# Kernel tuning notes

Hardware: AMD Instinct MI355X
Metric: run time of the kernel (lower is better)

The kernel has to match this reference:

```python
import jax, jax.numpy as jnp
import numpy as np

B, T, C = 8, 2048, 1024
EXP = 4
EPS = 1e-6


def rmsnorm(x, w):
    xf = x.astype(jnp.float32)
    y = xf * jax.lax.rsqrt(jnp.mean(xf * xf, axis=-1, keepdims=True) + EPS)
    return y.astype(x.dtype) * w


def setup_inputs() -> dict:
    key = jax.random.key(0)
    ks = jax.random.split(key, 8)
    x = jax.random.normal(ks[0], (B, T, C), dtype=jnp.float32)
    norm1_w = jnp.ones((C,), jnp.float32)
    norm2_w = jnp.ones((C,), jnp.float32)
    s1 = 1.0 / np.sqrt(C)
    s2 = 1.0 / np.sqrt(EXP * C)
    mlp1_w = jax.random.uniform(ks[1], (C, C), jnp.float32, -s1, s1)  # stored (in,out)
    mlp1_b = jax.random.uniform(ks[2], (C,), jnp.float32, -s1, s1)
    mlp2_w1 = jax.random.uniform(ks[3], (C, EXP * C), jnp.float32, -s1, s1)
    mlp2_b1 = jax.random.uniform(ks[4], (EXP * C,), jnp.float32, -s1, s1)
    mlp2_w2 = jax.random.uniform(ks[5], (EXP * C, C), jnp.float32, -s2, s2)
    mlp2_b2 = jax.random.uniform(ks[6], (C,), jnp.float32, -s2, s2)
    return {"x": x, "norm1_w": norm1_w, "mlp1_w": mlp1_w, "mlp1_b": mlp1_b,
            "norm2_w": norm2_w, "mlp2_w1": mlp2_w1, "mlp2_b1": mlp2_b1,
            "mlp2_w2": mlp2_w2, "mlp2_b2": mlp2_b2}


def reference(x, norm1_w, mlp1_w, mlp1_b, norm2_w, mlp2_w1, mlp2_b1, mlp2_w2, mlp2_b2):
    Tdim = x.shape[-2]
    # linear-RNN cumulative state with triangular-number scaler (faithful to source)
    state = jnp.cumsum(rmsnorm(x, norm1_w), axis=1)
    scaler = jnp.cumsum(jnp.arange(1, Tdim + 1, dtype=x.dtype))[None, :, None]
    state = state / scaler
    gate = jax.nn.sigmoid(jnp.einsum('btc,cd->btd', state, mlp1_w) + mlp1_b)
    out = gate * x
    h = rmsnorm(out, norm2_w)
    h = jax.nn.relu(jnp.einsum('btc,ce->bte', h, mlp2_w1) + mlp2_b1)
    out = jnp.einsum('bte,ec->btc', h, mlp2_w2) + mlp2_b2 + out
    return out
```

## Files before the change

### kernel.cpp

```cpp
#include <hip/hip_runtime.h>

__device__ __forceinline__ float bf2f(unsigned short u) {
    union { unsigned int i; float f; } v;
    v.i = ((unsigned int)u) << 16;
    return v.f;
}
__device__ __forceinline__ unsigned short f2bf(float f) {
    union { float f; unsigned int i; } v;
    v.f = f;
    unsigned int r = (v.i + 0x7fffu + ((v.i >> 16) & 1u)) >> 16;
    return (unsigned short)r;
}

typedef __attribute__((ext_vector_type(8))) short short8;
typedef __attribute__((ext_vector_type(4))) float floatx4;

#define GLOBAL_AS __attribute__((address_space(1)))
#define LDS_AS __attribute__((address_space(3)))

static constexpr int Bdim = 8;
static constexpr int Tdim = 2048;
static constexpr int Cdim = 1024;
static constexpr int Edim = 4096;
static constexpr int Mdim = Bdim * Tdim;

__global__ __launch_bounds__(256) void transpose_f2b(
    const float* __restrict__ src, unsigned short* __restrict__ dst, int K, int N) {
    __shared__ float tile[32][33];
    int n0 = blockIdx.x * 32;
    int k0 = blockIdx.y * 32;
    int tx = threadIdx.x & 31;
    int ty = threadIdx.x >> 5;
#pragma unroll
    for (int i = 0; i < 32; i += 8)
        tile[ty + i][tx] = src[(size_t)(k0 + ty + i) * N + n0 + tx];
    __syncthreads();
#pragma unroll
    for (int i = 0; i < 32; i += 8)
        dst[(size_t)(n0 + ty + i) * K + k0 + tx] = f2bf(tile[tx][ty + i]);
}

__global__ __launch_bounds__(256) void rms_inv_kernel(
    const float* __restrict__ x, float* __restrict__ rinv) {
    int row = blockIdx.x;
    int tid = threadIdx.x;
    float4 v = ((const float4*)(x + (size_t)row * Cdim))[tid];
    float s = v.x * v.x + v.y * v.y + v.z * v.z + v.w * v.w;
#pragma unroll
    for (int o = 32; o > 0; o >>= 1) s += __shfl_down(s, o, 64);
    __shared__ float ps[4];
    if ((tid & 63) == 0) ps[tid >> 6] = s;
    __syncthreads();
    if (tid == 0) {
        float tot = ps[0] + ps[1] + ps[2] + ps[3];
        rinv[row] = rsqrtf(tot * (1.0f / (float)Cdim) + 1e-6f);
    }
}

__global__ __launch_bounds__(256) void chunk_sums(
    const float* __restrict__ x, const float* __restrict__ rinv,
    const float* __restrict__ w, float* __restrict__ P) {
    int idx = blockIdx.x;
    int cb = idx & 3;
    int k = (idx >> 2) & 31;
    int b = idx >> 7;
    int c = cb * 256 + threadIdx.x;
    float wc = w[c];
    const float* base = x + ((size_t)b * Tdim + k * 64) * Cdim + c;
    const float* rbase = rinv + (size_t)b * Tdim + k * 64;
    float s = 0.f;
#pragma unroll 8
    for (int t = 0; t < 64; t++) s += base[(size_t)t * Cdim] * rbase[t];
    P[((size_t)b * 32 + k) * Cdim + c] = s * wc;
}

__global__ __launch_bounds__(256) void chunk_scan(float* __restrict__ P) {
    int g = blockIdx.x * 256 + threadIdx.x;
    int b = g >> 10;
    int c = g & 1023;
    float* p = P + (size_t)b * 32 * Cdim + c;
    float run = 0.f;
#pragma unroll
    for (int k = 0; k < 32; k++) {
        float v = p[(size_t)k * Cdim];
        p[(size_t)k * Cdim] = run;
        run += v;
    }
}

__global__ __launch_bounds__(256) void cumsum_state(
    const float* __restrict__ x, const float* __restrict__ rinv,
    const float* __restrict__ w, const float* __restrict__ P,
    unsigned short* __restrict__ state) {
    int idx = blockIdx.x;
    int cb = idx & 3;
    int k = (idx >> 2) & 31;
    int b = idx >> 7;
    int c = cb * 256 + threadIdx.x;
    float wc = w[c];
    float acc = P[((size_t)b * 32 + k) * Cdim + c];
    const float* base = x + ((size_t)b * Tdim + k * 64) * Cdim + c;
    const float* rbase = rinv + (size_t)b * Tdim + k * 64;
    unsigned short* sbase = state + ((size_t)b * Tdim + k * 64) * Cdim + c;
#pragma unroll 4
    for (int t = 0; t < 64; t++) {
        acc += base[(size_t)t * Cdim] * rbase[t] * wc;
        int tt = k * 64 + t;
        float inv = 2.0f / ((float)(tt + 1) * (float)(tt + 2));
        sbase[(size_t)t * Cdim] = f2bf(acc * inv);
    }
}

__global__ __launch_bounds__(256) void rmsnorm_f2b(
    const float* __restrict__ x, const float* __restrict__ w,
    unsigned short* __restrict__ y) {
    int row = blockIdx.x;
    int tid = threadIdx.x;
    float4 v = ((const float4*)(x + (size_t)row * Cdim))[tid];
    float s = v.x * v.x + v.y * v.y + v.z * v.z + v.w * v.w;
#pragma unroll
    for (int o = 32; o > 0; o >>= 1) s += __shfl_down(s, o, 64);
    __shared__ float ps[4];
    if ((tid & 63) == 0) ps[tid >> 6] = s;
    __syncthreads();
    float tot = ps[0] + ps[1] + ps[2] + ps[3];
    float r = rsqrtf(tot * (1.0f / (float)Cdim) + 1e-6f);
    float4 w4 = ((const float4*)w)[tid];
    ushort4 o;
    o.x = f2bf(v.x * r * w4.x);
    o.y = f2bf(v.y * r * w4.y);
    o.z = f2bf(v.z * r * w4.z);
    o.w = f2bf(v.w * r * w4.w);
    ((ushort4*)(y + (size_t)row * Cdim))[tid] = o;
}

template <int EPI>
__global__ __launch_bounds__(512, 2) void gemm8(
    const unsigned short* __restrict__ A, const unsigned short* __restrict__ BT,
    const float* __restrict__ bias, const float* __restrict__ extra,
    void* __restrict__ Coutv, int N, int K) {
    __shared__ __attribute__((aligned(16))) unsigned short As[3][256 * 64];
    __shared__ __attribute__((aligned(16))) unsigned short Bs[3][128 * 64];

    int tid = threadIdx.x;
    int nbn = N >> 7;
    int id = blockIdx.x;
    int nwg = gridDim.x;
    if ((nwg & 7) == 0) id = (id & 7) * (nwg >> 3) + (id >> 3);
    int bn = id % nbn;
    int bm = id / nbn;

    int lane = tid & 63;
    int w = tid >> 6;
    int wm = w & 3;
    int wn = w >> 2;
    int lrow = lane & 15;
    int l4 = lane >> 4;
    int swz = lrow & 7;

    const unsigned short* Abase = A + (size_t)bm * 256 * K;
    const unsigned short* Bbase = BT + (size_t)bn * 128 * K;

    int sr = tid >> 3;
    int col8 = (tid & 7) ^ (sr & 7);

#define STAGE_A(sb, u, k0)                                                               \
    __builtin_amdgcn_global_load_lds(                                                    \
        (const GLOBAL_AS void*)(Abase + (size_t)((u) * 64 + sr) * K + (k0) + col8 * 8),  \
        (LDS_AS void*)(As[sb] + (u) * 4096 + tid * 8), 16, 0, 0)
#define STAGE_B(sb, u, k0)                                                               \
    __builtin_amdgcn_global_load_lds(                                                    \
        (const GLOBAL_AS void*)(Bbase + (size_t)((u) * 64 + sr) * K + (k0) + col8 * 8),  \
        (LDS_AS void*)(Bs[sb] + (u) * 4096 + tid * 8), 16, 0, 0)

    floatx4 acc[4][4] = {};
    int nt = K >> 6;

    STAGE_A(0, 0, 0); STAGE_A(0, 1, 0); STAGE_A(0, 2, 0); STAGE_A(0, 3, 0);
    STAGE_B(0, 0, 0); STAGE_B(0, 1, 0);
    STAGE_A(1, 0, 64); STAGE_A(1, 1, 64); STAGE_A(1, 2, 64); STAGE_A(1, 3, 64);
    STAGE_B(1, 0, 64); STAGE_B(1, 1, 64);
    asm volatile("s_waitcnt vmcnt(6)" ::: "memory");
    __builtin_amdgcn_s_barrier();

    int buf = 0;
    for (int t = 0; t < nt; t++) {
        const unsigned short* Ab = As[buf];
        const unsigned short* Bb = Bs[buf];
        int sb = buf + 2; if (sb >= 3) sb -= 3;
        int k2 = (t + 2) << 6;
        bool st = (t + 2) < nt;

        short8 af[4][2], bfr[2][2];
#pragma unroll
        for (int i = 0; i < 4; i++)
#pragma unroll
            for (int ks = 0; ks < 2; ks++)
                af[i][ks] = *(const short8*)(Ab + (wm * 64 + i * 16 + lrow) * 64 +
                                             (((ks * 4 + l4) ^ swz) << 3));
#pragma unroll
        for (int j = 0; j < 2; j++)
#pragma unroll
            for (int ks = 0; ks < 2; ks++)
                bfr[j][ks] = *(const short8*)(Bb + (wn * 64 + j * 16 + lrow) * 64 +
                                              (((ks * 4 + l4) ^ swz) << 3));
        if (st) { STAGE_A(sb, 0, k2); STAGE_A(sb, 1, k2); STAGE_A(sb, 2, k2); }
        asm volatile("s_waitcnt lgkmcnt(8)" ::: "memory");
        __builtin_amdgcn_s_barrier();
        asm volatile("s_waitcnt lgkmcnt(0)" ::: "memory");
        __builtin_amdgcn_s_setprio(1);
#pragma unroll
        for (int i = 0; i < 4; i++)
#pragma unroll
            for (int j = 0; j < 2; j++)
#pragma unroll
                for (int ks = 0; ks < 2; ks++)
                    acc[i][j] = __builtin_amdgcn_mfma_f32_16x16x32_bf16(
                        af[i][ks], bfr[j][ks], acc[i][j], 0, 0, 0);
        __builtin_amdgcn_s_setprio(0);
        __builtin_amdgcn_s_barrier();

#pragma unroll
        for (int j = 0; j < 2; j++)
#pragma unroll
            for (int ks = 0; ks < 2; ks++)
                bfr[j][ks] = *(const short8*)(Bb + (wn * 64 + (j + 2) * 16 + lrow) * 64 +
                                              (((ks * 4 + l4) ^ swz) << 3));
        if (st) { STAGE_A(sb, 3, k2); STAGE_B(sb, 0, k2); STAGE_B(sb, 1, k2); }
        __builtin_amdgcn_s_barrier();
        asm volatile("s_waitcnt lgkmcnt(0)" ::: "memory");
        __builtin_amdgcn_s_setprio(1);
#pragma unroll
        for (int i = 0; i < 4; i++)
#pragma unroll
            for (int j = 0; j < 2; j++)
#pragma unroll
                for (int ks = 0; ks < 2; ks++)
                    acc[i][j + 2] = __builtin_amdgcn_mfma_f32_16x16x32_bf16(
                        af[i][ks], bfr[j][ks], acc[i][j + 2], 0, 0, 0);
        __builtin_amdgcn_s_setprio(0);
        if (t + 1 < nt) {
            if (st) asm volatile("s_waitcnt vmcnt(6)" ::: "memory");
            else    asm volatile("s_waitcnt vmcnt(0)" ::: "memory");
        }
        __builtin_amdgcn_s_barrier();

        buf++; if (buf == 3) buf = 0;
    }
#undef STAGE_A
#undef STAGE_B

    int crow = l4 << 2;
    int ccol = lane & 15;
#pragma unroll
    for (int i = 0; i < 4; i++) {
#pragma unroll
        for (int j = 0; j < 4; j++) {
            size_t gm = (size_t)bm * 256 + wm * 64 + i * 16 + crow;
            size_t gn = (size_t)bn * 128 + wn * 64 + j * 16 + ccol;
            float bsv = bias[gn];
#pragma unroll
            for (int r = 0; r < 4; r++) {
                float v = acc[i][j][r] + bsv;
                size_t off = (gm + r) * (size_t)N + gn;
                if (EPI == 0) {
                    float g = 1.f / (1.f + __expf(-v));
                    ((float*)Coutv)[off] = g * extra[off];
                } else if (EPI == 1) {
                    ((unsigned short*)Coutv)[off] = f2bf(v > 0.f ? v : 0.f);
                } else {
                    ((float*)Coutv)[off] = v + extra[off];
                }
            }
        }
    }
}

extern "C" void kernel_launch(void* const* d_in, const int* in_sizes, int n_in,
                              void* d_out, int out_size, void* d_ws, size_t ws_size,
                              hipStream_t stream) {
    const float* x   = (const float*)d_in[0];
    const float* n1w = (const float*)d_in[1];
    const float* w1  = (const float*)d_in[2];
    const float* b1  = (const float*)d_in[3];
    const float* n2w = (const float*)d_in[4];
    const float* w21 = (const float*)d_in[5];
    const float* b21 = (const float*)d_in[6];
    const float* w22 = (const float*)d_in[7];
    const float* b22 = (const float*)d_in[8];
    float* out = (float*)d_out;

    char* ws = (char*)d_ws;
    const size_t MB = 1024ull * 1024ull;
    unsigned short* state = (unsigned short*)(ws);
    unsigned short* w1T   = (unsigned short*)(ws + 32 * MB);
    unsigned short* w21T  = (unsigned short*)(ws + 34 * MB);
    unsigned short* w22T  = (unsigned short*)(ws + 42 * MB);
    float* P              = (float*)(ws + 50 * MB);
    float* rinv           = (float*)(ws + 51 * MB);
    unsigned short* h     = (unsigned short*)(ws + 52 * MB);
    float* out1 = out;

    int slice_rows = Mdim;
    while (52 * MB + (size_t)slice_rows * Edim * 2 > ws_size && slice_rows > 1024)
        slice_rows >>= 1;

    transpose_f2b<<<dim3(Cdim / 32, Cdim / 32), 256, 0, stream>>>(w1, w1T, Cdim, Cdim);
    transpose_f2b<<<dim3(Edim / 32, Cdim / 32), 256, 0, stream>>>(w21, w21T, Cdim, Edim);
    transpose_f2b<<<dim3(Cdim / 32, Edim / 32), 256, 0, stream>>>(w22, w22T, Edim, Cdim);

    rms_inv_kernel<<<Mdim, 256, 0, stream>>>(x, rinv);

    chunk_sums<<<1024, 256, 0, stream>>>(x, rinv, n1w, P);
    chunk_scan<<<32, 256, 0, stream>>>(P);
    cumsum_state<<<1024, 256, 0, stream>>>(x, rinv, n1w, P, state);

    gemm8<0><<<dim3((Mdim / 256) * (Cdim / 128)), 512, 0, stream>>>(
        state, w1T, b1, x, out1, Cdim, Cdim);

    rmsnorm_f2b<<<Mdim, 256, 0, stream>>>(out1, n2w, state);

    for (int m0 = 0; m0 < Mdim; m0 += slice_rows) {
        gemm8<1><<<dim3((slice_rows / 256) * (Edim / 128)), 512, 0, stream>>>(
            state + (size_t)m0 * Cdim, w21T, b21, nullptr, h, Edim, Cdim);
        gemm8<2><<<dim3((slice_rows / 256) * (Cdim / 128)), 512, 0, stream>>>(
            h, w22T, b22, out1 + (size_t)m0 * Cdim, out + (size_t)m0 * Cdim,
            Cdim, Edim);
    }
}
```

Baseline: 612.0 us.

## Enlarge GEMM tile to 256x256 with double-buffered 8-phase MFMA pipeline

```diff
diff --git a/kernel.cpp b/kernel.cpp
--- a/kernel.cpp
+++ b/kernel.cpp
@@ -139,11 +139,11 @@
     const unsigned short* __restrict__ A, const unsigned short* __restrict__ BT,
     const float* __restrict__ bias, const float* __restrict__ extra,
     void* __restrict__ Coutv, int N, int K) {
-    __shared__ __attribute__((aligned(16))) unsigned short As[3][256 * 64];
-    __shared__ __attribute__((aligned(16))) unsigned short Bs[3][128 * 64];
+    __shared__ __attribute__((aligned(16))) unsigned short As[2][256 * 64];
+    __shared__ __attribute__((aligned(16))) unsigned short Bs[2][256 * 64];
 
     int tid = threadIdx.x;
-    int nbn = N >> 7;
+    int nbn = N >> 8;
     int id = blockIdx.x;
     int nwg = gridDim.x;
     if ((nwg & 7) == 0) id = (id & 7) * (nwg >> 3) + (id >> 3);
@@ -152,14 +152,15 @@
 
     int lane = tid & 63;
     int w = tid >> 6;
-    int wm = w & 3;
-    int wn = w >> 2;
+    int wm = w >> 2;
+    int wn = w & 3;
     int lrow = lane & 15;
     int l4 = lane >> 4;
     int swz = lrow & 7;
+    int wmB = wm * 128, wnB = wn * 64;
 
     const unsigned short* Abase = A + (size_t)bm * 256 * K;
-    const unsigned short* Bbase = BT + (size_t)bn * 128 * K;
+    const unsigned short* Bbase = BT + (size_t)bn * 256 * K;
 
     int sr = tid >> 3;
     int col8 = (tid & 7) ^ (sr & 7);
@@ -173,95 +174,161 @@
         (const GLOBAL_AS void*)(Bbase + (size_t)((u) * 64 + sr) * K + (k0) + col8 * 8),  \
         (LDS_AS void*)(Bs[sb] + (u) * 4096 + tid * 8), 16, 0, 0)
 
-    floatx4 acc[4][4] = {};
+#define LDA(cb, i, ks)                                                                   \
+    (*(const short8*)(As[cb] + (wmB + (i) * 16 + lrow) * 64 + ((((ks) * 4 + l4) ^ swz) << 3)))
+#define LDB(cb, jj, ks)                                                                  \
+    (*(const short8*)(Bs[cb] + (wnB + (jj) * 16 + lrow) * 64 + ((((ks) * 4 + l4) ^ swz) << 3)))
+
+#define PH_IN                                                                            \
+    do {                                                                                 \
+        __builtin_amdgcn_s_barrier();                                                    \
+        asm volatile("s_waitcnt lgkmcnt(0)" ::: "memory");                               \
+        __builtin_amdgcn_s_setprio(1);                                                   \
+    } while (0)
+#define PH_OUT                                                                           \
+    do {                                                                                 \
+        __builtin_amdgcn_s_setprio(0);                                                   \
+        __builtin_amdgcn_s_barrier();                                                    \
+    } while (0)
+
+    floatx4 acc[8][4] = {};
     int nt = K >> 6;
+    int nIter = nt >> 1;
 
     STAGE_A(0, 0, 0); STAGE_A(0, 1, 0); STAGE_A(0, 2, 0); STAGE_A(0, 3, 0);
-    STAGE_B(0, 0, 0); STAGE_B(0, 1, 0);
-    STAGE_A(1, 0, 64); STAGE_A(1, 1, 64); STAGE_A(1, 2, 64); STAGE_A(1, 3, 64);
-    STAGE_B(1, 0, 64); STAGE_B(1, 1, 64);
-    asm volatile("s_waitcnt vmcnt(6)" ::: "memory");
+    STAGE_B(0, 0, 0); STAGE_B(0, 1, 0); STAGE_B(0, 2, 0); STAGE_B(0, 3, 0);
+    STAGE_B(1, 0, 64); STAGE_B(1, 1, 64); STAGE_B(1, 2, 64); STAGE_B(1, 3, 64);
+    asm volatile("s_waitcnt vmcnt(4)" ::: "memory");
     __builtin_amdgcn_s_barrier();
 
-    int buf = 0;
-    for (int t = 0; t < nt; t++) {
-        const unsigned short* Ab = As[buf];
-        const unsigned short* Bb = Bs[buf];
-        int sb = buf + 2; if (sb >= 3) sb -= 3;
-        int k2 = (t + 2) << 6;
-        bool st = (t + 2) < nt;
-
-        short8 af[4][2], bfr[2][2];
-#pragma unroll
-        for (int i = 0; i < 4; i++)
-#pragma unroll
-            for (int ks = 0; ks < 2; ks++)
-                af[i][ks] = *(const short8*)(Ab + (wm * 64 + i * 16 + lrow) * 64 +
-                                             (((ks * 4 + l4) ^ swz) << 3));
-#pragma unroll
-        for (int j = 0; j < 2; j++)
-#pragma unroll
-            for (int ks = 0; ks < 2; ks++)
-                bfr[j][ks] = *(const short8*)(Bb + (wn * 64 + j * 16 + lrow) * 64 +
-                                              (((ks * 4 + l4) ^ swz) << 3));
-        if (st) { STAGE_A(sb, 0, k2); STAGE_A(sb, 1, k2); STAGE_A(sb, 2, k2); }
-        asm volatile("s_waitcnt lgkmcnt(8)" ::: "memory");
+    for (int j = 0; j < nIter; ++j) {
+        int k1 = (2 * j + 1) << 6;
+        int k2 = (2 * j + 2) << 6;
+        int k3 = (2 * j + 3) << 6;
+        bool nl = (j + 1 < nIter);
+
+        short8 av[4], b0[4], b1[4];
+
+#pragma unroll
+        for (int i = 0; i < 4; i++) av[i] = LDA(0, i, 0);
+#pragma unroll
+        for (int i = 0; i < 4; i++) b0[i] = LDB(0, i, 0);
+        STAGE_A(1, 0, k1); STAGE_A(1, 1, k1);
+        PH_IN;
+#pragma unroll
+        for (int i = 0; i < 4; i++)
+#pragma unroll
+            for (int q = 0; q < 4; q++)
+                acc[i][q] = __builtin_amdgcn_mfma_f32_16x16x32_bf16(av[i], b0[q], acc[i][q], 0, 0, 0);
+        PH_OUT;
+
+#pragma unroll
+        for (int i = 0; i < 4; i++) av[i] = LDA(0, i, 1);
+#pragma unroll
+        for (int i = 0; i < 4; i++) b1[i] = LDB(0, i, 1);
+        STAGE_A(1, 2, k1); STAGE_A(1, 3, k1);
+        PH_IN;
+#pragma unroll
+        for (int i = 0; i < 4; i++)
+#pragma unroll
+            for (int q = 0; q < 4; q++)
+                acc[i][q] = __builtin_amdgcn_mfma_f32_16x16x32_bf16(av[i], b1[q], acc[i][q], 0, 0, 0);
+        PH_OUT;
+
+#pragma unroll
+        for (int i = 0; i < 4; i++) av[i] = LDA(0, 4 + i, 0);
+        if (nl) { STAGE_B(0, 0, k2); STAGE_B(0, 1, k2); }
+        PH_IN;
+#pragma unroll
+        for (int i = 0; i < 4; i++)
+#pragma unroll
+            for (int q = 0; q < 4; q++)
+                acc[4 + i][q] = __builtin_amdgcn_mfma_f32_16x16x32_bf16(av[i], b0[q], acc[4 + i][q], 0, 0, 0);
+        PH_OUT;
+
+#pragma unroll
+        for (int i = 0; i < 4; i++) av[i] = LDA(0, 4 + i, 1);
+        if (nl) { STAGE_B(0, 2, k2); STAGE_B(0, 3, k2); }
+        PH_IN;
+#pragma unroll
+        for (int i = 0; i < 4; i++)
+#pragma unroll
+            for (int q = 0; q < 4; q++)
+                acc[4 + i][q] = __builtin_amdgcn_mfma_f32_16x16x32_bf16(av[i], b1[q], acc[4 + i][q], 0, 0, 0);
+        __builtin_amdgcn_s_setprio(0);
+        if (nl) asm volatile("s_waitcnt vmcnt(4)" ::: "memory");
+        else    asm volatile("s_waitcnt vmcnt(0)" ::: "memory");
         __builtin_amdgcn_s_barrier();
-        asm volatile("s_waitcnt lgkmcnt(0)" ::: "memory");
-        __builtin_amdgcn_s_setprio(1);
-#pragma unroll
-        for (int i = 0; i < 4; i++)
-#pragma unroll
-            for (int j = 0; j < 2; j++)
-#pragma unroll
-                for (int ks = 0; ks < 2; ks++)
-                    acc[i][j] = __builtin_amdgcn_mfma_f32_16x16x32_bf16(
-                        af[i][ks], bfr[j][ks], acc[i][j], 0, 0, 0);
+
+#pragma unroll
+        for (int i = 0; i < 4; i++) av[i] = LDA(1, i, 0);
+#pragma unroll
+        for (int i = 0; i < 4; i++) b0[i] = LDB(1, i, 0);
+        if (nl) { STAGE_A(0, 0, k2); STAGE_A(0, 1, k2); }
+        PH_IN;
+#pragma unroll
+        for (int i = 0; i < 4; i++)
+#pragma unroll
+            for (int q = 0; q < 4; q++)
+                acc[i][q] = __builtin_amdgcn_mfma_f32_16x16x32_bf16(av[i], b0[q], acc[i][q], 0, 0, 0);
+        PH_OUT;
+
+#pragma unroll
+        for (int i = 0; i < 4; i++) av[i] = LDA(1, i, 1);
+#pragma unroll
+        for (int i = 0; i < 4; i++) b1[i] = LDB(1, i, 1);
+        if (nl) { STAGE_A(0, 2, k2); STAGE_A(0, 3, k2); }
+        PH_IN;
+#pragma unroll
+        for (int i = 0; i < 4; i++)
+#pragma unroll
+            for (int q = 0; q < 4; q++)
+                acc[i][q] = __builtin_amdgcn_mfma_f32_16x16x32_bf16(av[i], b1[q], acc[i][q], 0, 0, 0);
+        PH_OUT;
+
+#pragma unroll
+        for (int i = 0; i < 4; i++) av[i] = LDA(1, 4 + i, 0);
+        if (nl) { STAGE_B(1, 0, k3); STAGE_B(1, 1, k3); }
+        PH_IN;
+#pragma unroll
+        for (int i = 0; i < 4; i++)
+#pragma unroll
+            for (int q = 0; q < 4; q++)
+                acc[4 + i][q] = __builtin_amdgcn_mfma_f32_16x16x32_bf16(av[i], b0[q], acc[4 + i][q], 0, 0, 0);
+        PH_OUT;
+
+#pragma unroll
+        for (int i = 0; i < 4; i++) av[i] = LDA(1, 4 + i, 1);
+        if (nl) { STAGE_B(1, 2, k3); STAGE_B(1, 3, k3); }
+        PH_IN;
+#pragma unroll
+        for (int i = 0; i < 4; i++)
+#pragma unroll
+            for (int q = 0; q < 4; q++)
+                acc[4 + i][q] = __builtin_amdgcn_mfma_f32_16x16x32_bf16(av[i], b1[q], acc[4 + i][q], 0, 0, 0);
         __builtin_amdgcn_s_setprio(0);
+        if (nl) asm volatile("s_waitcnt vmcnt(4)" ::: "memory");
         __builtin_amdgcn_s_barrier();
-
-#pragma unroll
-        for (int j = 0; j < 2; j++)
-#pragma unroll
-            for (int ks = 0; ks < 2; ks++)
-                bfr[j][ks] = *(const short8*)(Bb + (wn * 64 + (j + 2) * 16 + lrow) * 64 +
-                                              (((ks * 4 + l4) ^ swz) << 3));
-        if (st) { STAGE_A(sb, 3, k2); STAGE_B(sb, 0, k2); STAGE_B(sb, 1, k2); }
-        __builtin_amdgcn_s_barrier();
-        asm volatile("s_waitcnt lgkmcnt(0)" ::: "memory");
-        __builtin_amdgcn_s_setprio(1);
-#pragma unroll
-        for (int i = 0; i < 4; i++)
-#pragma unroll
-            for (int j = 0; j < 2; j++)
-#pragma unroll
-                for (int ks = 0; ks < 2; ks++)
-                    acc[i][j + 2] = __builtin_amdgcn_mfma_f32_16x16x32_bf16(
-                        af[i][ks], bfr[j][ks], acc[i][j + 2], 0, 0, 0);
-        __builtin_amdgcn_s_setprio(0);
-        if (t + 1 < nt) {
-            if (st) asm volatile("s_waitcnt vmcnt(6)" ::: "memory");
-            else    asm volatile("s_waitcnt vmcnt(0)" ::: "memory");
-        }
-        __builtin_amdgcn_s_barrier();
-
-        buf++; if (buf == 3) buf = 0;
     }
 #undef STAGE_A
 #undef STAGE_B
+#undef LDA
+#undef LDB
+#undef PH_IN
+#undef PH_OUT
 
     int crow = l4 << 2;
     int ccol = lane & 15;
 #pragma unroll
-    for (int i = 0; i < 4; i++) {
-#pragma unroll
-        for (int j = 0; j < 4; j++) {
-            size_t gm = (size_t)bm * 256 + wm * 64 + i * 16 + crow;
-            size_t gn = (size_t)bn * 128 + wn * 64 + j * 16 + ccol;
+    for (int i = 0; i < 8; i++) {
+#pragma unroll
+        for (int q = 0; q < 4; q++) {
+            size_t gm = (size_t)bm * 256 + wmB + i * 16 + crow;
+            size_t gn = (size_t)bn * 256 + wnB + q * 16 + ccol;
             float bsv = bias[gn];
 #pragma unroll
             for (int r = 0; r < 4; r++) {
-                float v = acc[i][j][r] + bsv;
+                float v = acc[i][q][r] + bsv;
                 size_t off = (gm + r) * (size_t)N + gn;
                 if (EPI == 0) {
                     float g = 1.f / (1.f + __expf(-v));
@@ -315,15 +382,15 @@
     chunk_scan<<<32, 256, 0, stream>>>(P);
     cumsum_state<<<1024, 256, 0, stream>>>(x, rinv, n1w, P, state);
 
-    gemm8<0><<<dim3((Mdim / 256) * (Cdim / 128)), 512, 0, stream>>>(
+    gemm8<0><<<dim3((Mdim / 256) * (Cdim / 256)), 512, 0, stream>>>(
         state, w1T, b1, x, out1, Cdim, Cdim);
 
     rmsnorm_f2b<<<Mdim, 256, 0, stream>>>(out1, n2w, state);
 
     for (int m0 = 0; m0 < Mdim; m0 += slice_rows) {
-        gemm8<1><<<dim3((slice_rows / 256) * (Edim / 128)), 512, 0, stream>>>(
+        gemm8<1><<<dim3((slice_rows / 256) * (Edim / 256)), 512, 0, stream>>>(
             state + (size_t)m0 * Cdim, w21T, b21, nullptr, h, Edim, Cdim);
-        gemm8<2><<<dim3((slice_rows / 256) * (Cdim / 128)), 512, 0, stream>>>(
+        gemm8<2><<<dim3((slice_rows / 256) * (Cdim / 256)), 512, 0, stream>>>(
             h, w22T, b22, out1 + (size_t)m0 * Cdim, out + (size_t)m0 * Cdim,
             Cdim, Edim);
     }
```

New measurement: 561.8 us. -8.2%, faster.
